# Optimization experiments

Measured on AMD Instinct MI355X. Metric: run time of the kernel, lower is better.

Reference implementation:

```python
import jax, jax.numpy as jnp
import numpy as np

IN_FEATURES = 4096
OUT_FEATURES = 4096
SPARSE_RATIO = 0.1
NNZ = int(IN_FEATURES * OUT_FEATURES * SPARSE_RATIO)  # 1677721
N_COLS = 4096  # x is (out_features, N); bias broadcast requires N == out_features


def setup_inputs() -> dict:
    key = jax.random.key(0)
    k_x, k_r, k_c, k_v, k_b = jax.random.split(key, 5)
    x = jax.random.normal(k_x, (OUT_FEATURES, N_COLS), dtype=jnp.float32)
    rows = jax.random.randint(k_r, (NNZ,), 0, IN_FEATURES, dtype=jnp.int32)
    cols = jax.random.randint(k_c, (NNZ,), 0, OUT_FEATURES, dtype=jnp.int32)
    vals = jax.random.normal(k_v, (NNZ,), dtype=jnp.float32)
    bias = jax.random.normal(k_b, (OUT_FEATURES,), dtype=jnp.float32)
    return {"x": x, "rows": rows, "cols": cols, "vals": vals, "bias": bias}


def reference(x, rows, cols, vals, bias):
    # Scatter the COO weight into its dense form once (duplicate coords
    # accumulate, matching sparse COO coalescing semantics), then do a
    # dense GEMM: y = W @ x + bias. Same math as torch.sparse.mm.
    W = jnp.zeros((IN_FEATURES, OUT_FEATURES), dtype=x.dtype).at[rows, cols].add(vals)
    return W @ x + bias  # (in_features, N) + (out_features,) broadcast on last axis
```

## Files before the change

kernel.cpp:

```cpp
#include <hip/hip_runtime.h>
#include <stdint.h>

#define MDIM 4096
#define NDIM 4096
#define KDIM 4096

typedef float f32x4 __attribute__((ext_vector_type(4)));
typedef __bf16 bf16x8 __attribute__((ext_vector_type(8)));
typedef short s16x8 __attribute__((ext_vector_type(8)));


__device__ __forceinline__ unsigned short f2bf(float x) {
  union { float f; unsigned u; } v; v.f = x;
  return (unsigned short)((v.u + 0x7fffu + ((v.u >> 16) & 1u)) >> 16);
}
__device__ __forceinline__ float bf2f(unsigned short b) {
  union { unsigned u; float f; } v; v.u = ((unsigned)b) << 16;
  return v.f;
}

__global__ void scatter_kernel(const int* __restrict__ rows, const int* __restrict__ cols,
                               const float* __restrict__ vals, unsigned* __restrict__ Wb,
                               int nnz) {
  int i = blockIdx.x * blockDim.x + threadIdx.x;
  if (i >= nnz) return;
  int m = rows[i], k = cols[i];
  float v = vals[i];
  size_t chunk = ((((size_t)(m >> 7) * 128 + (k >> 5)) * 8 + ((m >> 4) & 7)) * 64) +
                 (((k >> 3) & 3) * 16 + (m & 15));
  size_t idx = chunk * 8 + (k & 7);
  unsigned* word = &Wb[idx >> 1];
  unsigned shift = (idx & 1) ? 16u : 0u;
  unsigned old = *word, assumed;
  do {
    assumed = old;
    unsigned short cur = (unsigned short)(assumed >> shift);
    unsigned short upd = f2bf(bf2f(cur) + v);
    unsigned next = (assumed & ~(0xffffu << shift)) | ((unsigned)upd << shift);
    if (next == assumed) break;
    old = atomicCAS(word, assumed, next);
  } while (old != assumed);
}

__global__ __launch_bounds__(256) void packx_kernel(const float* __restrict__ x,
                                                    short* __restrict__ Bpk) {
  __shared__ float tile[32 * 65];
  int tid = threadIdx.x;
  int n0 = blockIdx.x * 64, k0 = blockIdx.y * 32;
#pragma unroll
  for (int r = 0; r < 8; r++) {
    int elem = r * 256 + tid;
    int kk = elem >> 6, nn = elem & 63;
    tile[kk * 65 + nn] = x[(size_t)(k0 + kk) * NDIM + n0 + nn];
  }
  __syncthreads();
  int region = tid >> 6, lane = tid & 63;
  int kh = lane >> 4, nl = region * 16 + (lane & 15);
  s16x8 v;
#pragma unroll
  for (int j = 0; j < 8; j++) v[j] = (short)f2bf(tile[(kh * 8 + j) * 65 + nl]);
  int f = ((n0 & 127) >> 4) + region;
  size_t chunk = (((size_t)(n0 >> 7) * 128 + (k0 >> 5)) * 8 + f) * 64 + lane;
  *(s16x8*)&Bpk[chunk * 8] = v;
}

__global__ __launch_bounds__(256) void gemm_kernel(const short* __restrict__ A,
                                                   const short* __restrict__ Bt,
                                                   const float* __restrict__ bias,
                                                   float* __restrict__ C) {
  __shared__ __align__(16) short sA[2][128 * 32];
  __shared__ __align__(16) short sB[2][128 * 32];
  int tid = threadIdx.x, lane = tid & 63, wave = tid >> 6;
  int wr = wave >> 1, wc = wave & 1;
  int m16 = lane & 15, quad = lane >> 4;
  int rowBase = blockIdx.y * 128, colBase = blockIdx.x * 128;

  f32x4 acc[4][4];
#pragma unroll
  for (int i = 0; i < 4; i++)
#pragma unroll
    for (int j = 0; j < 4; j++) acc[i][j] = f32x4{0.f, 0.f, 0.f, 0.f};

  const short* aSrc[2];
  const short* bSrc[2];
  int ldsDst[2];
#pragma unroll
  for (int s = 0; s < 2; s++) {
    int f = wave + s * 4;
    aSrc[s] = A + ((size_t)blockIdx.y * 128 * 8 + f) * 512 + lane * 8;
    bSrc[s] = Bt + ((size_t)blockIdx.x * 128 * 8 + f) * 512 + lane * 8;
    ldsDst[s] = f * 512;
  }

#pragma unroll
  for (int s = 0; s < 2; s++) {
    __builtin_amdgcn_global_load_lds(
        (const __attribute__((address_space(1))) void*)aSrc[s],
        (__attribute__((address_space(3))) void*)&sA[0][ldsDst[s]], 16, 0, 0);
    __builtin_amdgcn_global_load_lds(
        (const __attribute__((address_space(1))) void*)bSrc[s],
        (__attribute__((address_space(3))) void*)&sB[0][ldsDst[s]], 16, 0, 0);
  }

#pragma unroll 2
  for (int it = 0; it < 128; it++) {
    int buf = it & 1, nxt = buf ^ 1;
    int tnext = (it + 1) & 127;
#pragma unroll
    for (int s = 0; s < 2; s++) {
      __builtin_amdgcn_global_load_lds(
          (const __attribute__((address_space(1))) void*)(aSrc[s] + (size_t)tnext * 4096),
          (__attribute__((address_space(3))) void*)&sA[nxt][ldsDst[s]], 16, 0, 0);
      __builtin_amdgcn_global_load_lds(
          (const __attribute__((address_space(1))) void*)(bSrc[s] + (size_t)tnext * 4096),
          (__attribute__((address_space(3))) void*)&sB[nxt][ldsDst[s]], 16, 0, 0);
    }
    __builtin_amdgcn_s_waitcnt(0x0F74);
    __builtin_amdgcn_s_barrier();

    bf16x8 a[4], b[4];
#pragma unroll
    for (int i = 0; i < 4; i++)
      a[i] = *(const bf16x8*)&sA[buf][((wr * 4 + i) * 64 + lane) * 8];
#pragma unroll
    for (int j = 0; j < 4; j++)
      b[j] = *(const bf16x8*)&sB[buf][((wc * 4 + j) * 64 + lane) * 8];
#pragma unroll
    for (int i = 0; i < 4; i++)
#pragma unroll
      for (int j = 0; j < 4; j++)
        acc[i][j] = __builtin_amdgcn_mfma_f32_16x16x32_bf16(a[i], b[j], acc[i][j], 0, 0, 0);

    __builtin_amdgcn_s_waitcnt(0xC07F);
    __builtin_amdgcn_s_barrier();
  }
  __builtin_amdgcn_s_waitcnt(0x0F70);

#pragma unroll
  for (int j = 0; j < 4; j++) {
    int col = colBase + wc * 64 + j * 16 + m16;
    float bv = bias[col];
#pragma unroll
    for (int i = 0; i < 4; i++) {
      int row0 = rowBase + wr * 64 + i * 16 + quad * 4;
      f32x4 v = acc[i][j];
#pragma unroll
      for (int r = 0; r < 4; r++) C[(size_t)(row0 + r) * NDIM + col] = v[r] + bv;
    }
  }
}

extern "C" void kernel_launch(void* const* d_in, const int* in_sizes, int n_in,
                              void* d_out, int out_size, void* d_ws, size_t ws_size,
                              hipStream_t stream) {
  const float* x = (const float*)d_in[0];
  const int* rows = (const int*)d_in[1];
  const int* cols = (const int*)d_in[2];
  const float* vals = (const float*)d_in[3];
  const float* bias = (const float*)d_in[4];
  int nnz = in_sizes[1];
  float* y = (float*)d_out;

  char* ws = (char*)d_ws;
  short* Wpk = (short*)ws;
  short* Xpk = (short*)(ws + (32u << 20));

  hipMemsetAsync(Wpk, 0, (size_t)MDIM * KDIM * sizeof(short), stream);
  scatter_kernel<<<(nnz + 255) / 256, 256, 0, stream>>>(rows, cols, vals, (unsigned*)Wpk, nnz);
  packx_kernel<<<dim3(NDIM / 64, KDIM / 32), 256, 0, stream>>>(x, Xpk);
  gemm_kernel<<<dim3(NDIM / 128, MDIM / 128), 256, 0, stream>>>(Wpk, Xpk, bias, y);
}
```

Measured before the change: 381.3 us.

## Fuse scatter and x-packing into one prep kernel with packed bf16 atomics

Merges the COO scatter and the x transpose/pack kernels into a single launch, where block index selects the role. The scatter now uses a hardware packed bf16x2 atomic add (unsafeAtomicAdd on __hip_bfloat162) when available, with the CAS loop kept as a fallback. This removes one kernel launch and lets the two prep phases overlap. It also replaces a CAS retry loop with a single atomic. Converting each value to bf16 before adding changes the rounding slightly, and the shared-memory tile is now allocated for scatter blocks too, which may lower their occupancy.

```diff
diff --git a/kernel.cpp b/kernel.cpp
--- a/kernel.cpp
+++ b/kernel.cpp
@@ -1,4 +1,5 @@
 #include <hip/hip_runtime.h>
+#include <hip/hip_bf16.h>
 #include <stdint.h>
 
 #define MDIM 4096
@@ -19,18 +20,10 @@
   return v.f;
 }
 
-__global__ void scatter_kernel(const int* __restrict__ rows, const int* __restrict__ cols,
-                               const float* __restrict__ vals, unsigned* __restrict__ Wb,
-                               int nnz) {
-  int i = blockIdx.x * blockDim.x + threadIdx.x;
-  if (i >= nnz) return;
-  int m = rows[i], k = cols[i];
-  float v = vals[i];
-  size_t chunk = ((((size_t)(m >> 7) * 128 + (k >> 5)) * 8 + ((m >> 4) & 7)) * 64) +
-                 (((k >> 3) & 3) * 16 + (m & 15));
-  size_t idx = chunk * 8 + (k & 7);
-  unsigned* word = &Wb[idx >> 1];
-  unsigned shift = (idx & 1) ? 16u : 0u;
+__device__ __forceinline__ void cas_add_bf16(unsigned short* addr2, unsigned short bits, int hi) {
+  unsigned* word = (unsigned*)addr2;
+  unsigned shift = hi ? 16u : 0u;
+  float v = bf2f(bits);
   unsigned old = *word, assumed;
   do {
     assumed = old;
@@ -42,26 +35,66 @@
   } while (old != assumed);
 }
 
-__global__ __launch_bounds__(256) void packx_kernel(const float* __restrict__ x,
-                                                    short* __restrict__ Bpk) {
-  __shared__ float tile[32 * 65];
-  int tid = threadIdx.x;
-  int n0 = blockIdx.x * 64, k0 = blockIdx.y * 32;
-#pragma unroll
-  for (int r = 0; r < 8; r++) {
-    int elem = r * 256 + tid;
-    int kk = elem >> 6, nn = elem & 63;
-    tile[kk * 65 + nn] = x[(size_t)(k0 + kk) * NDIM + n0 + nn];
-  }
-  __syncthreads();
-  int region = tid >> 6, lane = tid & 63;
-  int kh = lane >> 4, nl = region * 16 + (lane & 15);
-  s16x8 v;
-#pragma unroll
-  for (int j = 0; j < 8; j++) v[j] = (short)f2bf(tile[(kh * 8 + j) * 65 + nl]);
-  int f = ((n0 & 127) >> 4) + region;
-  size_t chunk = (((size_t)(n0 >> 7) * 128 + (k0 >> 5)) * 8 + f) * 64 + lane;
-  *(s16x8*)&Bpk[chunk * 8] = v;
+template <typename T>
+__device__ __forceinline__ auto pk_add_impl(T* p, T v, int)
+    -> decltype(unsafeAtomicAdd(p, v), void()) {
+  unsafeAtomicAdd(p, v);
+}
+template <typename T>
+__device__ __forceinline__ void pk_add_impl(T* p, T v, long) {
+  union { T t; unsigned u; } c; c.t = v;
+  unsigned short lo = (unsigned short)(c.u & 0xffffu);
+  unsigned short hi16 = (unsigned short)(c.u >> 16);
+  if (lo) cas_add_bf16((unsigned short*)p, lo, 0);
+  if (hi16) cas_add_bf16((unsigned short*)p, hi16, 1);
+}
+
+__device__ __forceinline__ void atomic_bf16_add(unsigned short* base2, unsigned short bits, int hi) {
+  __hip_bfloat162_raw raw;
+  raw.x = hi ? (unsigned short)0 : bits;
+  raw.y = hi ? bits : (unsigned short)0;
+  __hip_bfloat162 v(raw);
+  pk_add_impl((__hip_bfloat162*)base2, v, 0);
+}
+
+__global__ __launch_bounds__(256) void prep_kernel(const int* __restrict__ rows,
+                                                   const int* __restrict__ cols,
+                                                   const float* __restrict__ vals, int nnz,
+                                                   int scBlocks,
+                                                   unsigned short* __restrict__ Wpk,
+                                                   const float* __restrict__ x,
+                                                   short* __restrict__ Xpk) {
+  int b = blockIdx.x, tid = threadIdx.x;
+  if (b < scBlocks) {
+    int i = b * 256 + tid;
+    if (i >= nnz) return;
+    int m = rows[i], k = cols[i];
+    unsigned short bits = f2bf(vals[i]);
+    size_t chunk = ((((size_t)(m >> 7) * 128 + (k >> 5)) * 8 + ((m >> 4) & 7)) * 64) +
+                   (((k >> 3) & 3) * 16 + (m & 15));
+    size_t idx = chunk * 8 + (k & 7);
+    atomic_bf16_add(&Wpk[idx & ~(size_t)1], bits, (int)(idx & 1));
+  } else {
+    __shared__ float tile[32 * 65];
+    int pb = b - scBlocks;
+    int n0 = (pb & 63) * 64, k0 = (pb >> 6) * 32;
+#pragma unroll
+    for (int r = 0; r < 8; r++) {
+      int elem = r * 256 + tid;
+      int kk = elem >> 6, nn = elem & 63;
+      tile[kk * 65 + nn] = x[(size_t)(k0 + kk) * NDIM + n0 + nn];
+    }
+    __syncthreads();
+    int region = tid >> 6, lane = tid & 63;
+    int kh = lane >> 4, nl = region * 16 + (lane & 15);
+    s16x8 v;
+#pragma unroll
+    for (int j = 0; j < 8; j++) v[j] = (short)f2bf(tile[(kh * 8 + j) * 65 + nl]);
+    int f = region;
+    f = ((n0 & 127) >> 4) + region;
+    size_t chunk = (((size_t)(n0 >> 7) * 128 + (k0 >> 5)) * 8 + f) * 64 + lane;
+    *(s16x8*)&Xpk[chunk * 8] = v;
+  }
 }
 
 __global__ __launch_bounds__(256) void gemm_kernel(const short* __restrict__ A,
@@ -162,11 +195,14 @@
   float* y = (float*)d_out;
 
   char* ws = (char*)d_ws;
-  short* Wpk = (short*)ws;
+  unsigned short* Wpk = (unsigned short*)ws;
   short* Xpk = (short*)(ws + (32u << 20));
 
+  int scBlocks = (nnz + 255) / 256;
+  int pxBlocks = (NDIM / 64) * (KDIM / 32);
+
   hipMemsetAsync(Wpk, 0, (size_t)MDIM * KDIM * sizeof(short), stream);
-  scatter_kernel<<<(nnz + 255) / 256, 256, 0, stream>>>(rows, cols, vals, (unsigned*)Wpk, nnz);
-  packx_kernel<<<dim3(NDIM / 64, KDIM / 32), 256, 0, stream>>>(x, Xpk);
-  gemm_kernel<<<dim3(NDIM / 128, MDIM / 128), 256, 0, stream>>>(Wpk, Xpk, bias, y);
-}
+  prep_kernel<<<scBlocks + pxBlocks, 256, 0, stream>>>(rows, cols, vals, nnz, scBlocks,
+                                                       Wpk, x, Xpk);
+  gemm_kernel<<<dim3(NDIM / 128, MDIM / 128), 256, 0, stream>>>((const short*)Wpk, Xpk, bias, y);
+}
```

New measurement: 366.6 us. 1.04x faster.
